# Optimization experiments

Measured on AMD Instinct MI355X. Metric: run time of the kernel, lower is better.

## Reference

```python
import jax, jax.numpy as jnp
import numpy as np

STRIDES = (8.0, 16.0, 32.0)
ANCHORS = np.array([[[12,16],[19,36],[40,28]],
                    [[36,75],[76,55],[72,146]],
                    [[142,110],[192,243],[459,401]]], dtype=np.float32)  # [3 levels, 3 anchors, 2] in input pixels
INPUT_SIZE = 416.0
IGNORE_THRESHOLD = 0.5
EPS = 1e-7
MAX_BOXES = 64  # fixed cap on true boxes per image for jit-able ignore-mask
NC = 80


def _bce_logits(logits, targets):
    # numerically-stable binary cross entropy with logits, elementwise
    return jnp.maximum(logits, 0.0) - logits * targets + jnp.log1p(jnp.exp(-jnp.abs(logits)))


def _iou_xywh(b1, b2):
    # center-format boxes, broadcastable; returns IoU over last dim pair
    a1 = b1[..., 2] * b1[..., 3]
    a2 = b2[..., 2] * b2[..., 3]
    lt = jnp.maximum(b1[..., :2] - b1[..., 2:] * 0.5, b2[..., :2] - b2[..., 2:] * 0.5)
    rb = jnp.minimum(b1[..., :2] + b1[..., 2:] * 0.5, b2[..., :2] + b2[..., 2:] * 0.5)
    wh = jnp.maximum(rb - lt, 0.0)
    inter = wh[..., 0] * wh[..., 1]
    union = a1 + a2 - inter
    return inter / jnp.maximum(union, 1e-9)


def _level_loss(feature, label, idx):
    N, C, H, W = feature.shape
    f = feature.transpose(0, 2, 3, 1).reshape(N, H, W, 3, -1)
    raw_xy, raw_wh = f[..., 0:2], f[..., 2:4]
    raw_conf, raw_prob = f[..., 4:5], f[..., 5:]

    label_xywh = label[..., 0:4]
    label_conf = label[..., 4:5]
    label_prob = label[..., 5:]

    stride = STRIDES[idx]
    anchors = jnp.asarray(ANCHORS[idx])  # [3,2]

    gy, gx = jnp.meshgrid(jnp.arange(H, dtype=f.dtype), jnp.arange(W, dtype=f.dtype), indexing='ij')
    grid = jnp.stack([gx, gy], axis=-1)[:, :, None, :]  # [H,W,1,2]

    # decode predictions (GeneratePrediction)
    pred_xy = (jax.nn.sigmoid(raw_xy) + grid) * stride
    pred_wh = jnp.exp(raw_wh) * anchors
    pred_xywh = jnp.concatenate([pred_xy, pred_wh], axis=-1)  # [N,H,W,3,4]

    xy_offset = label_xywh[..., :2] / stride - grid
    wh_offset = label_conf * jnp.log(label_xywh[..., 2:4] / anchors + EPS)
    bbox_loss_scale = 2.0 - label_xywh[..., 2:3] * label_xywh[..., 3:4] / (INPUT_SIZE * INPUT_SIZE)

    # ignore mask: max IoU of each prediction against this image's true boxes
    conf_flat = label_conf[..., 0].reshape(N, -1)          # [N, H*W*3]
    boxes_flat = label_xywh.reshape(N, -1, 4)              # [N, H*W*3, 4]
    k = min(MAX_BOXES, conf_flat.shape[1])
    vals, idxs = jax.lax.top_k(conf_flat, k)               # positives first (conf is 0/1)
    true_boxes = jnp.take_along_axis(boxes_flat, idxs[..., None], axis=1)  # [N,k,4]
    valid = vals > 0.0                                     # [N,k]
    iou = _iou_xywh(pred_xywh[..., None, :], true_boxes[:, None, None, None, :, :])  # [N,H,W,3,k]
    iou = jnp.where(valid[:, None, None, None, :], iou, 0.0)
    max_iou = jnp.max(iou, axis=-1)                        # [N,H,W,3]; 0 when no valid boxes
    ignore_mask = (max_iou < IGNORE_THRESHOLD).astype(f.dtype)[..., None]

    xy_loss = label_conf * bbox_loss_scale * _bce_logits(raw_xy, xy_offset)
    wh_loss = label_conf * bbox_loss_scale * 0.5 * jnp.square(raw_wh - wh_offset)
    bce_conf = _bce_logits(raw_conf, label_conf)
    conf_loss = label_conf * bce_conf + (1.0 - label_conf) * ignore_mask * bce_conf
    prob_loss = label_conf * _bce_logits(raw_prob, label_prob)

    sum_axes = (1, 2, 3, 4)
    reg = jnp.mean(jnp.sum(xy_loss, axis=sum_axes)) + jnp.mean(jnp.sum(wh_loss, axis=sum_axes))
    conf = jnp.mean(jnp.sum(conf_loss, axis=sum_axes))
    prob = jnp.mean(jnp.sum(prob_loss, axis=sum_axes))
    return reg, conf, prob


def _make_label(key, N, H, W, p_pos):
    kc, kxy, kwh, kp = jax.random.split(key, 4)
    conf = (jax.random.uniform(kc, (N, H, W, 3, 1)) < p_pos).astype(jnp.float32)
    xy = jax.random.uniform(kxy, (N, H, W, 3, 2)) * INPUT_SIZE
    wh = jax.random.uniform(kwh, (N, H, W, 3, 2)) * 190.0 + 10.0  # strictly positive
    prob = (jax.random.uniform(kp, (N, H, W, 3, NC)) < 0.0125).astype(jnp.float32)
    return jnp.concatenate([xy, wh, conf, prob], axis=-1)


def setup_inputs() -> dict:
    key = jax.random.key(0)
    ks = jax.random.split(key, 6)
    N, C = 16, 3 * (5 + NC)
    sizes = [52, 26, 13]
    preds = [jax.random.normal(ks[i], (N, C, s, s), dtype=jnp.float32) for i, s in enumerate(sizes)]
    labels = [_make_label(ks[3 + i], N, s, s, 0.0008) for i, s in enumerate(sizes)]
    return {"pred0": preds[0], "pred1": preds[1], "pred2": preds[2],
            "label0": labels[0], "label1": labels[1], "label2": labels[2]}


def reference(pred0, pred1, pred2, label0, label1, label2):
    reg = conf = prob = 0.0
    for i, (f, l) in enumerate([(pred0, label0), (pred1, label1), (pred2, label2)]):
        r, c, p = _level_loss(f, l, i)
        reg, conf, prob = reg + r, conf + c, prob + p
    return (reg, conf, prob)
```

## Files before the change

kernel.cpp:

```cpp
#include <hip/hip_runtime.h>


#define NIMG 16
#define MAXB 64

#define C0 (16 * 3 * 52 * 52)
#define C1 (16 * 3 * 26 * 26)
#define C2 (16 * 3 * 13 * 13)
#define CTOT (C0 + C1 + C2)
#define NBLK ((CTOT + 255) / 256)
#define NPOS 48
#define NALL (NBLK + NPOS)

#define WS_COUNTS   0
#define WS_BOXES    256
#define WS_CELLIDS  49408
#define WS_PARTIAL  65536

__device__ __constant__ float d_anchors[3][3][2] = {
    {{12.f, 16.f}, {19.f, 36.f}, {40.f, 28.f}},
    {{36.f, 75.f}, {76.f, 55.f}, {72.f, 146.f}},
    {{142.f, 110.f}, {192.f, 243.f}, {459.f, 401.f}}};

__device__ __forceinline__ float bce_logits(float x, float t) {
    return fmaxf(x, 0.f) - x * t + log1pf(expf(-fabsf(x)));
}

__global__ void scan_labels(const float* __restrict__ l0,
                            const float* __restrict__ l1,
                            const float* __restrict__ l2,
                            int* __restrict__ counts,
                            float4* __restrict__ boxes,
                            int* __restrict__ cellids) {
    int rec = blockIdx.x * blockDim.x + threadIdx.x;
    if (rec >= CTOT) return;

    const float* lab;
    int level, cell, hw3;
    if (rec < C0)           { level = 0; cell = rec;           lab = l0; hw3 = 3 * 52 * 52; }
    else if (rec < C0 + C1) { level = 1; cell = rec - C0;      lab = l1; hw3 = 3 * 26 * 26; }
    else                    { level = 2; cell = rec - C0 - C1; lab = l2; hw3 = 3 * 13 * 13; }

    const float* lp = lab + (size_t)cell * 85;
    float c = lp[4];
    if (c > 0.f) {
        int n = cell / hw3;
        int p = atomicAdd(&counts[level * NIMG + n], 1);
        if (p < MAXB) {
            float4 b;
            b.x = lp[0]; b.y = lp[1]; b.z = lp[2]; b.w = lp[3];
            boxes[(level * NIMG + n) * MAXB + p] = b;
            cellids[(level * NIMG + n) * MAXB + p] = cell;
        }
    }
}

__global__ __launch_bounds__(256) void loss_fused(
        const float* __restrict__ f0,
        const float* __restrict__ f1,
        const float* __restrict__ f2,
        const float* __restrict__ l0,
        const float* __restrict__ l1,
        const float* __restrict__ l2,
        const int* __restrict__ counts,
        const float4* __restrict__ boxes,
        const int* __restrict__ cellids,
        float* __restrict__ partial) {
    int lane = threadIdx.x & 63;
    int wid = threadIdx.x >> 6;

    if (blockIdx.x < NPOS) {
        int pb = blockIdx.x;
        int lv = pb / NIMG;
        int n = pb % NIMG;
        const float *f, *lab;
        int Wp, HWp; float strp;
        if (lv == 0)      { f = f0; lab = l0; Wp = 52; HWp = 52 * 52; strp = 8.f; }
        else if (lv == 1) { f = f1; lab = l1; Wp = 26; HWp = 26 * 26; strp = 16.f; }
        else              { f = f2; lab = l2; Wp = 13; HWp = 13 * 13; strp = 32.f; }

        int m = counts[pb];
        if (m > MAXB) m = MAXB;
        int bbase = pb * MAXB;

        float reg_acc = 0.f, prob_acc = 0.f;
        for (int i = wid; i < m; i += 4) {
            int pcell = cellids[bbase + i];
            float4 b = boxes[bbase + i];
            int a = pcell % 3;
            int hw = (pcell / 3) % HWp;
            int w = hw % Wp;
            int h = hw / Wp;
            const float* fp = f + ((size_t)n * 255 + (size_t)a * 85) * HWp + hw;
            const float* lp = lab + (size_t)pcell * 85;

            int ch1 = (lane < 40) ? (5 + lane) : ((lane < 44) ? (lane - 40) : 0);
            float g1 = fp[(size_t)ch1 * HWp];
            float g2 = fp[(size_t)((lane < 40) ? (45 + lane) : 0) * HWp];
            float t1 = lp[(lane < 40) ? (5 + lane) : 0];
            float t2 = lp[(lane < 40) ? (45 + lane) : 0];

            float pp = (lane < 40) ? (bce_logits(g1, t1) + bce_logits(g2, t2)) : 0.f;
            for (int off = 32; off > 0; off >>= 1) pp += __shfl_down(pp, off);

            float prx = __shfl(g1, 40);
            float pry = __shfl(g1, 41);
            float prw = __shfl(g1, 42);
            float prh = __shfl(g1, 43);
            if (lane == 0) {
                prob_acc += pp;
                float aw = d_anchors[lv][a][0];
                float ah = d_anchors[lv][a][1];
                float ox = b.x / strp - (float)w;
                float oy = b.y / strp - (float)h;
                float ow = logf(b.z / aw + 1e-7f);
                float oh = logf(b.w / ah + 1e-7f);
                float scale = 2.f - b.z * b.w * (1.f / (416.f * 416.f));
                float dw = prw - ow, dh = prh - oh;
                reg_acc += scale * (bce_logits(prx, ox) + bce_logits(pry, oy))
                         + scale * 0.5f * (dw * dw + dh * dh);
            }
        }
        __shared__ float sp[2][4];
        if (lane == 0) { sp[0][wid] = reg_acc; sp[1][wid] = prob_acc; }
        __syncthreads();
        if (threadIdx.x == 0) {
            partial[0 * 1024 + pb] = sp[0][0] + sp[0][1] + sp[0][2] + sp[0][3];
            partial[2 * 1024 + pb] = sp[1][0] + sp[1][1] + sp[1][2] + sp[1][3];
        }
    } else {
        int cb = blockIdx.x - NPOS;
        int gid = cb * blockDim.x + threadIdx.x;
        float conf = 0.f;

        if (gid < CTOT) {
            const float* f;
            int level, cell, W, HW;
            float stride;
            if (gid < C0)           { level = 0; cell = gid;           f = f0; W = 52; HW = 52 * 52; stride = 8.f; }
            else if (gid < C0 + C1) { level = 1; cell = gid - C0;      f = f1; W = 26; HW = 26 * 26; stride = 16.f; }
            else                    { level = 2; cell = gid - C0 - C1; f = f2; W = 13; HW = 13 * 13; stride = 32.f; }

            int hw = cell % HW;
            int na = cell / HW;
            int a = na % 3;
            int n = na / 3;
            int w = hw % W;
            int h = hw / W;
            int cell_lab = (n * HW + hw) * 3 + a;

            const float* fp = f + (size_t)n * 255 * HW + (size_t)a * 85 * HW + hw;
            float rx = fp[0];
            float ry = fp[HW];
            float rw = fp[2 * HW];
            float rh = fp[3 * HW];
            float rc = fp[4 * HW];

            float aw = d_anchors[level][a][0];
            float ah = d_anchors[level][a][1];
            float px = (1.f / (1.f + expf(-rx)) + (float)w) * stride;
            float py = (1.f / (1.f + expf(-ry)) + (float)h) * stride;
            float pw = expf(rw) * aw;
            float ph = expf(rh) * ah;

            int m = counts[level * NIMG + n];
            if (m > MAXB) m = MAXB;
            int base = (level * NIMG + n) * MAXB;
            float parea = pw * ph;
            float pl = px - pw * 0.5f, pr = px + pw * 0.5f;
            float pt = py - ph * 0.5f, pb = py + ph * 0.5f;
            float maxiou = 0.f;
            bool ispos = false;
            for (int i = 0; i < m; ++i) {
                float4 b = boxes[base + i];
                if (cellids[base + i] == cell_lab) ispos = true;
                float tl = b.x - b.z * 0.5f, tr = b.x + b.z * 0.5f;
                float tt = b.y - b.w * 0.5f, tb = b.y + b.w * 0.5f;
                float iw = fmaxf(fminf(pr, tr) - fmaxf(pl, tl), 0.f);
                float ih = fmaxf(fminf(pb, tb) - fmaxf(pt, tt), 0.f);
                float inter = iw * ih;
                float uni = parea + b.z * b.w - inter;
                float iou = inter / fmaxf(uni, 1e-9f);
                maxiou = fmaxf(maxiou, iou);
            }
            if (ispos)              conf = bce_logits(rc, 1.f);
            else if (maxiou < 0.5f) conf = bce_logits(rc, 0.f);
        }

        for (int off = 32; off > 0; off >>= 1) conf += __shfl_down(conf, off);
        __shared__ float sc[4];
        if (lane == 0) sc[wid] = conf;
        __syncthreads();
        if (threadIdx.x == 0)
            partial[1 * 1024 + cb] = sc[0] + sc[1] + sc[2] + sc[3];
    }
}

__global__ void finalize(const float* __restrict__ partial,
                         float* __restrict__ out) {
    float a0 = 0.f, a1 = 0.f, a2 = 0.f;
    for (int i = threadIdx.x; i < NBLK; i += 256) {
        a1 += partial[1 * 1024 + i];
        if (i < NPOS) {
            a0 += partial[0 * 1024 + i];
            a2 += partial[2 * 1024 + i];
        }
    }
    for (int off = 32; off > 0; off >>= 1) {
        a0 += __shfl_down(a0, off);
        a1 += __shfl_down(a1, off);
        a2 += __shfl_down(a2, off);
    }
    __shared__ float s[3][4];
    int lane = threadIdx.x & 63;
    int wid = threadIdx.x >> 6;
    if (lane == 0) { s[0][wid] = a0; s[1][wid] = a1; s[2][wid] = a2; }
    __syncthreads();
    if (threadIdx.x == 0) {
        out[0] = (s[0][0] + s[0][1] + s[0][2] + s[0][3]) * (1.f / 16.f);
        out[1] = (s[1][0] + s[1][1] + s[1][2] + s[1][3]) * (1.f / 16.f);
        out[2] = (s[2][0] + s[2][1] + s[2][2] + s[2][3]) * (1.f / 16.f);
    }
}

extern "C" void kernel_launch(void* const* d_in, const int* in_sizes, int n_in,
                              void* d_out, int out_size, void* d_ws, size_t ws_size,
                              hipStream_t stream) {
    const float* f0 = (const float*)d_in[0];
    const float* f1 = (const float*)d_in[1];
    const float* f2 = (const float*)d_in[2];
    const float* l0 = (const float*)d_in[3];
    const float* l1 = (const float*)d_in[4];
    const float* l2 = (const float*)d_in[5];
    float* out = (float*)d_out;

    int*    counts  = (int*)((char*)d_ws + WS_COUNTS);
    float4* boxes   = (float4*)((char*)d_ws + WS_BOXES);
    int*    cellids = (int*)((char*)d_ws + WS_CELLIDS);
    float*  partial = (float*)((char*)d_ws + WS_PARTIAL);

    hipMemsetAsync(d_ws, 0, 256, stream);

    scan_labels<<<NBLK, 256, 0, stream>>>(l0, l1, l2, counts, boxes, cellids);
    loss_fused<<<NALL, 256, 0, stream>>>(f0, f1, f2, l0, l1, l2,
                                         counts, boxes, cellids, partial);
    finalize<<<1, 256, 0, stream>>>(partial, out);
}
```

Baseline: 133.3 us.

## Fuse label scan into loss kernel with per-image completion counters

Removes the separate label-scan kernel and folds it into the fused loss kernel. Each block scans its own label cells, then releases a per-image 'done' counter, and spins until every image it covers is fully scanned before running the IoU and positive-loss work. This removes one kernel launch and the grid-wide barrier between the two kernels, and lets feature loads overlap with the scan. It depends on all blocks being co-resident (hinted by launch bounds of 3 blocks per CU), otherwise the spin-waits could deadlock; it also adds atomic and spin overhead.

```diff
diff --git a/kernel.cpp b/kernel.cpp
--- a/kernel.cpp
+++ b/kernel.cpp
@@ -12,9 +12,14 @@
 #define NPOS 48
 #define NALL (NBLK + NPOS)
 
+#define CPI0 (3 * 52 * 52)
+#define CPI1 (3 * 26 * 26)
+#define CPI2 (3 * 13 * 13)
+
 #define WS_COUNTS   0
-#define WS_BOXES    256
-#define WS_CELLIDS  49408
+#define WS_DONE     192
+#define WS_BOXES    512
+#define WS_CELLIDS  (512 + 48 * 64 * 16)
 #define WS_PARTIAL  65536
 
 __device__ __constant__ float d_anchors[3][3][2] = {
@@ -26,58 +31,151 @@
     return fmaxf(x, 0.f) - x * t + log1pf(expf(-fabsf(x)));
 }
 
-__global__ void scan_labels(const float* __restrict__ l0,
-                            const float* __restrict__ l1,
-                            const float* __restrict__ l2,
-                            int* __restrict__ counts,
-                            float4* __restrict__ boxes,
-                            int* __restrict__ cellids) {
-    int rec = blockIdx.x * blockDim.x + threadIdx.x;
-    if (rec >= CTOT) return;
-
-    const float* lab;
-    int level, cell, hw3;
-    if (rec < C0)           { level = 0; cell = rec;           lab = l0; hw3 = 3 * 52 * 52; }
-    else if (rec < C0 + C1) { level = 1; cell = rec - C0;      lab = l1; hw3 = 3 * 26 * 26; }
-    else                    { level = 2; cell = rec - C0 - C1; lab = l2; hw3 = 3 * 13 * 13; }
-
-    const float* lp = lab + (size_t)cell * 85;
-    float c = lp[4];
-    if (c > 0.f) {
-        int n = cell / hw3;
-        int p = atomicAdd(&counts[level * NIMG + n], 1);
-        if (p < MAXB) {
-            float4 b;
-            b.x = lp[0]; b.y = lp[1]; b.z = lp[2]; b.w = lp[3];
-            boxes[(level * NIMG + n) * MAXB + p] = b;
-            cellids[(level * NIMG + n) * MAXB + p] = cell;
-        }
-    }
-}
-
-__global__ __launch_bounds__(256) void loss_fused(
+__device__ __forceinline__ int li_cells(int li) {
+    int lv = li >> 4;
+    return lv == 0 ? CPI0 : (lv == 1 ? CPI1 : CPI2);
+}
+__device__ __forceinline__ int li_of(int g) {
+    if (g < C0) return g / CPI0;
+    if (g < C0 + C1) return 16 + (g - C0) / CPI1;
+    return 32 + (g - C0 - C1) / CPI2;
+}
+__device__ __forceinline__ int li_start(int li) {
+    int lv = li >> 4, n = li & 15;
+    if (lv == 0) return n * CPI0;
+    if (lv == 1) return C0 + n * CPI1;
+    return C0 + C1 + n * CPI2;
+}
+
+__global__ __launch_bounds__(256, 3) void yolo_fused(
         const float* __restrict__ f0,
         const float* __restrict__ f1,
         const float* __restrict__ f2,
         const float* __restrict__ l0,
         const float* __restrict__ l1,
         const float* __restrict__ l2,
-        const int* __restrict__ counts,
-        const float4* __restrict__ boxes,
-        const int* __restrict__ cellids,
+        int* __restrict__ counts,
+        int* __restrict__ done,
+        float4* __restrict__ boxes,
+        int* __restrict__ cellids,
         float* __restrict__ partial) {
-    int lane = threadIdx.x & 63;
-    int wid = threadIdx.x >> 6;
-
-    if (blockIdx.x < NPOS) {
-        int pb = blockIdx.x;
-        int lv = pb / NIMG;
-        int n = pb % NIMG;
+    if (blockIdx.x < NBLK) {
+        int gid = blockIdx.x * 256 + threadIdx.x;
+        bool act = gid < CTOT;
+
+        if (act) {
+            const float* lab; int lcell, cpi, libase;
+            if (gid < C0)           { lab = l0; lcell = gid;           cpi = CPI0; libase = 0;  }
+            else if (gid < C0 + C1) { lab = l1; lcell = gid - C0;      cpi = CPI1; libase = 16; }
+            else                    { lab = l2; lcell = gid - C0 - C1; cpi = CPI2; libase = 32; }
+            const float* lp = lab + (size_t)lcell * 85;
+            float c = lp[4];
+            if (c > 0.f) {
+                int li = libase + lcell / cpi;
+                int p = atomicAdd(&counts[li], 1);
+                if (p < MAXB) {
+                    float4 b;
+                    b.x = lp[0]; b.y = lp[1]; b.z = lp[2]; b.w = lp[3];
+                    boxes[li * MAXB + p] = b;
+                    cellids[li * MAXB + p] = lcell;
+                }
+            }
+        }
+        __syncthreads();
+
+        int s = blockIdx.x * 256;
+        int e = min(s + 256, CTOT);
+        int liA = li_of(s), liB = li_of(e - 1);
+        if (threadIdx.x == 0) {
+            if (liA == liB) {
+                __hip_atomic_fetch_add(&done[liA], e - s, __ATOMIC_RELEASE, __HIP_MEMORY_SCOPE_AGENT);
+            } else {
+                int b = li_start(liB);
+                __hip_atomic_fetch_add(&done[liA], b - s, __ATOMIC_RELEASE, __HIP_MEMORY_SCOPE_AGENT);
+                __hip_atomic_fetch_add(&done[liB], e - b, __ATOMIC_RELEASE, __HIP_MEMORY_SCOPE_AGENT);
+            }
+        }
+
+        int level = 0, W = 52, HW = 2704; float stride = 8.f;
+        const float* f = f0; int lvbase = 0;
+        if (gid >= C0 + C1)  { level = 2; f = f2; W = 13; HW = 169; stride = 32.f; lvbase = C0 + C1; }
+        else if (gid >= C0)  { level = 1; f = f1; W = 26; HW = 676; stride = 16.f; lvbase = C0; }
+        int cell = act ? gid - lvbase : 0;
+        int hw = cell % HW, na = cell / HW;
+        int a = na % 3, n = na / 3;
+        int w = hw % W, h = hw / W;
+        float rc = 0.f, px = 0.f, py = 0.f, pw = 0.f, ph = 0.f;
+        if (act) {
+            const float* fp = f + (size_t)n * 255 * HW + (size_t)a * 85 * HW + hw;
+            float rx = fp[0];
+            float ry = fp[HW];
+            float rw_ = fp[2 * HW];
+            float rh = fp[3 * HW];
+            rc = fp[4 * HW];
+            px = (1.f / (1.f + expf(-rx)) + (float)w) * stride;
+            py = (1.f / (1.f + expf(-ry)) + (float)h) * stride;
+            pw = expf(rw_) * d_anchors[level][a][0];
+            ph = expf(rh) * d_anchors[level][a][1];
+        }
+        float parea = pw * ph;
+        float pl = px - pw * 0.5f, pr = px + pw * 0.5f;
+        float pt = py - ph * 0.5f, pbm = py + ph * 0.5f;
+        int cell_lab = (n * HW + hw) * 3 + a;
+        int li = level * NIMG + n;
+
+        if (threadIdx.x == 0) {
+            while (__hip_atomic_load(&done[liA], __ATOMIC_RELAXED, __HIP_MEMORY_SCOPE_AGENT) < li_cells(liA))
+                __builtin_amdgcn_s_sleep(1);
+            if (liB != liA)
+                while (__hip_atomic_load(&done[liB], __ATOMIC_RELAXED, __HIP_MEMORY_SCOPE_AGENT) < li_cells(liB))
+                    __builtin_amdgcn_s_sleep(1);
+        }
+        __syncthreads();
+        __builtin_amdgcn_fence(__ATOMIC_ACQUIRE, "agent");
+
+        float conf = 0.f;
+        if (act) {
+            int m = counts[li];
+            if (m > MAXB) m = MAXB;
+            int bbase = li * MAXB;
+            float maxiou = 0.f;
+            bool ispos = false;
+            for (int i = 0; i < m; ++i) {
+                float4 b = boxes[bbase + i];
+                if (cellids[bbase + i] == cell_lab) ispos = true;
+                float tl = b.x - b.z * 0.5f, tr = b.x + b.z * 0.5f;
+                float tt = b.y - b.w * 0.5f, tb = b.y + b.w * 0.5f;
+                float iw = fmaxf(fminf(pr, tr) - fmaxf(pl, tl), 0.f);
+                float ih = fmaxf(fminf(pbm, tb) - fmaxf(pt, tt), 0.f);
+                float inter = iw * ih;
+                float uni = parea + b.z * b.w - inter;
+                maxiou = fmaxf(maxiou, inter / fmaxf(uni, 1e-9f));
+            }
+            if (ispos)              conf = bce_logits(rc, 1.f);
+            else if (maxiou < 0.5f) conf = bce_logits(rc, 0.f);
+        }
+        int lane = threadIdx.x & 63, wid = threadIdx.x >> 6;
+        for (int off = 32; off > 0; off >>= 1) conf += __shfl_down(conf, off);
+        __shared__ float scr[4];
+        if (lane == 0) scr[wid] = conf;
+        __syncthreads();
+        if (threadIdx.x == 0)
+            partial[1 * 1024 + blockIdx.x] = scr[0] + scr[1] + scr[2] + scr[3];
+    } else {
+        int pb = blockIdx.x - NBLK;
+        int lane = threadIdx.x & 63, wid = threadIdx.x >> 6;
+        int lv = pb / NIMG, n = pb % NIMG;
         const float *f, *lab;
         int Wp, HWp; float strp;
         if (lv == 0)      { f = f0; lab = l0; Wp = 52; HWp = 52 * 52; strp = 8.f; }
         else if (lv == 1) { f = f1; lab = l1; Wp = 26; HWp = 26 * 26; strp = 16.f; }
         else              { f = f2; lab = l2; Wp = 13; HWp = 13 * 13; strp = 32.f; }
+
+        if (threadIdx.x == 0)
+            while (__hip_atomic_load(&done[pb], __ATOMIC_RELAXED, __HIP_MEMORY_SCOPE_AGENT) < li_cells(pb))
+                __builtin_amdgcn_s_sleep(1);
+        __syncthreads();
+        __builtin_amdgcn_fence(__ATOMIC_ACQUIRE, "agent");
 
         int m = counts[pb];
         if (m > MAXB) m = MAXB;
@@ -128,71 +226,6 @@
             partial[0 * 1024 + pb] = sp[0][0] + sp[0][1] + sp[0][2] + sp[0][3];
             partial[2 * 1024 + pb] = sp[1][0] + sp[1][1] + sp[1][2] + sp[1][3];
         }
-    } else {
-        int cb = blockIdx.x - NPOS;
-        int gid = cb * blockDim.x + threadIdx.x;
-        float conf = 0.f;
-
-        if (gid < CTOT) {
-            const float* f;
-            int level, cell, W, HW;
-            float stride;
-            if (gid < C0)           { level = 0; cell = gid;           f = f0; W = 52; HW = 52 * 52; stride = 8.f; }
-            else if (gid < C0 + C1) { level = 1; cell = gid - C0;      f = f1; W = 26; HW = 26 * 26; stride = 16.f; }
-            else                    { level = 2; cell = gid - C0 - C1; f = f2; W = 13; HW = 13 * 13; stride = 32.f; }
-
-            int hw = cell % HW;
-            int na = cell / HW;
-            int a = na % 3;
-            int n = na / 3;
-            int w = hw % W;
-            int h = hw / W;
-            int cell_lab = (n * HW + hw) * 3 + a;
-
-            const float* fp = f + (size_t)n * 255 * HW + (size_t)a * 85 * HW + hw;
-            float rx = fp[0];
-            float ry = fp[HW];
-            float rw = fp[2 * HW];
-            float rh = fp[3 * HW];
-            float rc = fp[4 * HW];
-
-            float aw = d_anchors[level][a][0];
-            float ah = d_anchors[level][a][1];
-            float px = (1.f / (1.f + expf(-rx)) + (float)w) * stride;
-            float py = (1.f / (1.f + expf(-ry)) + (float)h) * stride;
-            float pw = expf(rw) * aw;
-            float ph = expf(rh) * ah;
-
-            int m = counts[level * NIMG + n];
-            if (m > MAXB) m = MAXB;
-            int base = (level * NIMG + n) * MAXB;
-            float parea = pw * ph;
-            float pl = px - pw * 0.5f, pr = px + pw * 0.5f;
-            float pt = py - ph * 0.5f, pb = py + ph * 0.5f;
-            float maxiou = 0.f;
-            bool ispos = false;
-            for (int i = 0; i < m; ++i) {
-                float4 b = boxes[base + i];
-                if (cellids[base + i] == cell_lab) ispos = true;
-                float tl = b.x - b.z * 0.5f, tr = b.x + b.z * 0.5f;
-                float tt = b.y - b.w * 0.5f, tb = b.y + b.w * 0.5f;
-                float iw = fmaxf(fminf(pr, tr) - fmaxf(pl, tl), 0.f);
-                float ih = fmaxf(fminf(pb, tb) - fmaxf(pt, tt), 0.f);
-                float inter = iw * ih;
-                float uni = parea + b.z * b.w - inter;
-                float iou = inter / fmaxf(uni, 1e-9f);
-                maxiou = fmaxf(maxiou, iou);
-            }
-            if (ispos)              conf = bce_logits(rc, 1.f);
-            else if (maxiou < 0.5f) conf = bce_logits(rc, 0.f);
-        }
-
-        for (int off = 32; off > 0; off >>= 1) conf += __shfl_down(conf, off);
-        __shared__ float sc[4];
-        if (lane == 0) sc[wid] = conf;
-        __syncthreads();
-        if (threadIdx.x == 0)
-            partial[1 * 1024 + cb] = sc[0] + sc[1] + sc[2] + sc[3];
     }
 }
 
@@ -235,14 +268,14 @@
     float* out = (float*)d_out;
 
     int*    counts  = (int*)((char*)d_ws + WS_COUNTS);
+    int*    done    = (int*)((char*)d_ws + WS_DONE);
     float4* boxes   = (float4*)((char*)d_ws + WS_BOXES);
     int*    cellids = (int*)((char*)d_ws + WS_CELLIDS);
     float*  partial = (float*)((char*)d_ws + WS_PARTIAL);
 
-    hipMemsetAsync(d_ws, 0, 256, stream);
-
-    scan_labels<<<NBLK, 256, 0, stream>>>(l0, l1, l2, counts, boxes, cellids);
-    loss_fused<<<NALL, 256, 0, stream>>>(f0, f1, f2, l0, l1, l2,
-                                         counts, boxes, cellids, partial);
+    hipMemsetAsync(d_ws, 0, 512, stream);
+
+    yolo_fused<<<NALL, 256, 0, stream>>>(f0, f1, f2, l0, l1, l2,
+                                         counts, done, boxes, cellids, partial);
     finalize<<<1, 256, 0, stream>>>(partial, out);
 }
```

After: 194.3 us. +45.8%, slower.
